# Performance work log

Hardware: AMD Instinct MI355X
Metric: run time of the kernel (lower is better)

## Reference

```python
import jax, jax.numpy as jnp
import numpy as np

BN_EPS = 1e-5

def setup_inputs() -> dict:
    key = jax.random.key(0)
    ks = jax.random.split(key, 6)
    N, D, H = 1024, 256, 128
    scale = 0.05
    return {
        "graph_embeddings": jax.random.normal(ks[0], (N, D), jnp.float32),
        "W1": jax.random.normal(ks[1], (2 * D, H), jnp.float32) * scale,
        "b1": jnp.zeros((H,), jnp.float32),
        "W2": jax.random.normal(ks[2], (H, 1), jnp.float32) * scale,
        "b2": jnp.zeros((1,), jnp.float32),
        "Wg": jax.random.normal(ks[3], (D, H), jnp.float32) * scale,
        "bg": jnp.zeros((H,), jnp.float32),
        "gamma": jnp.ones((H,), jnp.float32),
        "beta": jnp.zeros((H,), jnp.float32),
    }

def reference(graph_embeddings, W1, b1, W2, b2, Wg, bg, gamma, beta):
    N, D = graph_embeddings.shape
    # Pairwise similarity MLP: sim(i,j) = sigmoid(W2 @ relu(W1 @ [x_i; x_j] + b1) + b2)
    # Split W1 over the concat dim so we never materialize [N,N,2D].
    a = graph_embeddings @ W1[:D]          # [N, H] contribution of x_i
    c = graph_embeddings @ W1[D:]          # [N, H] contribution of x_j
    h = jax.nn.relu(a[:, None, :] + c[None, :, :] + b1)   # [N, N, H]
    sim = jax.nn.sigmoid(jnp.einsum('ijh,h->ij', h, W2[:, 0]) + b2[0])  # [N, N]
    # Torch loop uses sim(i,j) with i<j for both directions; keep edge iff sim > 0.5.
    U = jnp.triu(sim, k=1)
    A = jnp.where(U > 0.5, U, 0.0)
    A = A + A.T + jnp.eye(N, dtype=sim.dtype)  # symmetric + GCN self-loops (weight 1)
    # GCN symmetric normalization: D^{-1/2} A D^{-1/2}
    deg = A.sum(axis=1)
    dis = jax.lax.rsqrt(deg)
    A_hat = A * dis[:, None] * dis[None, :]
    out = A_hat @ (graph_embeddings @ Wg) + bg  # [N, H]
    # BatchNorm1d (training mode: batch stats, biased variance)
    mean = out.mean(axis=0)
    var = out.var(axis=0)
    out = gamma * (out - mean) * jax.lax.rsqrt(var + BN_EPS) + beta
    return jax.nn.relu(out)
```

## Files before the change

### kernel.cpp

```cpp
#include <hip/hip_runtime.h>
#include <math.h>

constexpr int NN = 1024;
constexpr int DD = 256;
constexpr int HH = 128;
constexpr float BN_EPS = 1e-5f;

constexpr int OFF_A      = 0;
constexpr int OFF_AP     = OFF_A + NN * NN;
constexpr int OFF_CP     = OFF_AP + NN * HH;
constexpr int OFF_Y      = OFF_CP + NN * HH;
constexpr int OFF_DEG    = OFF_Y + NN * HH;
constexpr int OFF_STATS  = OFF_DEG + NN;
constexpr int OFF_OUTPRE = OFF_STATS + 256;

__global__ __launch_bounds__(256) void k1_gemm(
    const float* __restrict__ X, const float* __restrict__ W1,
    const float* __restrict__ Wg, const float* __restrict__ b1,
    float* __restrict__ aP, float* __restrict__ cP, float* __restrict__ Y,
    float* __restrict__ deg, float* __restrict__ stats) {
  const int tid = threadIdx.x;
  const int blk = blockIdx.x;
  if (blk >= 192) {
    if (blk == 192) {
      for (int i = tid; i < NN; i += 256) deg[i] = 0.f;
    } else {
      stats[tid] = 0.f;
    }
    return;
  }
  __shared__ float xs[16 * 256];
  __shared__ float ws[64 * 128];
  const int i0 = (blk & 63) * 16;
  const int m = blk >> 6;
  const float* W = (m == 0) ? W1 : (m == 1 ? W1 + DD * HH : Wg);
  const float* Xbase = X + i0 * DD;
#pragma unroll
  for (int v = 0; v < 4; ++v) {
    const int fi = (v * 256 + tid) * 4;
    *(float4*)(xs + fi) = *(const float4*)(Xbase + fi);
  }
  const int tx = tid & 31, ty = tid >> 5;
  float4 acc0 = make_float4(0.f, 0.f, 0.f, 0.f);
  float4 acc1 = make_float4(0.f, 0.f, 0.f, 0.f);
  for (int c = 0; c < 4; ++c) {
    __syncthreads();
    const float* Wbase = W + c * 64 * HH;
#pragma unroll
    for (int v = 0; v < 8; ++v) {
      const int fi = (v * 256 + tid) * 4;
      *(float4*)(ws + fi) = *(const float4*)(Wbase + fi);
    }
    __syncthreads();
    const float* xr0 = xs + (ty * 2) * 256 + c * 64;
    const float* xr1 = xs + (ty * 2 + 1) * 256 + c * 64;
#pragma unroll 4
    for (int d = 0; d < 64; d += 4) {
      const float4 x0 = *(const float4*)(xr0 + d);
      const float4 x1 = *(const float4*)(xr1 + d);
      const float4 w0 = *(const float4*)(ws + (d + 0) * 128 + tx * 4);
      const float4 w1 = *(const float4*)(ws + (d + 1) * 128 + tx * 4);
      const float4 w2 = *(const float4*)(ws + (d + 2) * 128 + tx * 4);
      const float4 w3 = *(const float4*)(ws + (d + 3) * 128 + tx * 4);
      acc0.x = fmaf(x0.x, w0.x, acc0.x); acc0.y = fmaf(x0.x, w0.y, acc0.y);
      acc0.z = fmaf(x0.x, w0.z, acc0.z); acc0.w = fmaf(x0.x, w0.w, acc0.w);
      acc1.x = fmaf(x1.x, w0.x, acc1.x); acc1.y = fmaf(x1.x, w0.y, acc1.y);
      acc1.z = fmaf(x1.x, w0.z, acc1.z); acc1.w = fmaf(x1.x, w0.w, acc1.w);
      acc0.x = fmaf(x0.y, w1.x, acc0.x); acc0.y = fmaf(x0.y, w1.y, acc0.y);
      acc0.z = fmaf(x0.y, w1.z, acc0.z); acc0.w = fmaf(x0.y, w1.w, acc0.w);
      acc1.x = fmaf(x1.y, w1.x, acc1.x); acc1.y = fmaf(x1.y, w1.y, acc1.y);
      acc1.z = fmaf(x1.y, w1.z, acc1.z); acc1.w = fmaf(x1.y, w1.w, acc1.w);
      acc0.x = fmaf(x0.z, w2.x, acc0.x); acc0.y = fmaf(x0.z, w2.y, acc0.y);
      acc0.z = fmaf(x0.z, w2.z, acc0.z); acc0.w = fmaf(x0.z, w2.w, acc0.w);
      acc1.x = fmaf(x1.z, w2.x, acc1.x); acc1.y = fmaf(x1.z, w2.y, acc1.y);
      acc1.z = fmaf(x1.z, w2.z, acc1.z); acc1.w = fmaf(x1.z, w2.w, acc1.w);
      acc0.x = fmaf(x0.w, w3.x, acc0.x); acc0.y = fmaf(x0.w, w3.y, acc0.y);
      acc0.z = fmaf(x0.w, w3.z, acc0.z); acc0.w = fmaf(x0.w, w3.w, acc0.w);
      acc1.x = fmaf(x1.w, w3.x, acc1.x); acc1.y = fmaf(x1.w, w3.y, acc1.y);
      acc1.z = fmaf(x1.w, w3.z, acc1.z); acc1.w = fmaf(x1.w, w3.w, acc1.w);
    }
  }
  float* dst = (m == 0) ? aP : (m == 1 ? cP : Y);
  if (m == 0) {
    const float4 bv = *(const float4*)(b1 + tx * 4);
    acc0.x += bv.x; acc0.y += bv.y; acc0.z += bv.z; acc0.w += bv.w;
    acc1.x += bv.x; acc1.y += bv.y; acc1.z += bv.z; acc1.w += bv.w;
  }
  const int r0 = i0 + ty * 2;
  *(float4*)(dst + r0 * HH + tx * 4) = acc0;
  *(float4*)(dst + (r0 + 1) * HH + tx * 4) = acc1;
}

__global__ __launch_bounds__(256) void k2_pairwise(
    const float* __restrict__ aP, const float* __restrict__ cP,
    const float* __restrict__ W2, const float* __restrict__ b2,
    float* __restrict__ A, float* __restrict__ deg) {
  __shared__ float as[32 * 132];
  __shared__ float cs[32 * 132];
  __shared__ float es[32 * 33];
  __shared__ float ws2[128];
  const int tid = threadIdx.x;
  int tt = blockIdx.x, ti = 0;
  while (tt >= 32 - ti) { tt -= 32 - ti; ++ti; }
  const int tj = ti + tt;
  const int i0 = ti * 32, j0 = tj * 32;
  if (tid < 32) *(float4*)(ws2 + tid * 4) = *(const float4*)(W2 + tid * 4);
  for (int idx = tid; idx < 32 * HH; idx += 256) {
    const int row = idx >> 7, col = idx & 127;
    as[row * 132 + col] = aP[(i0 + row) * HH + col];
    cs[row * 132 + col] = cP[(j0 + row) * HH + col];
  }
  __syncthreads();
  const int li0 = (tid >> 4) * 2, lj0 = (tid & 15) * 2;
  float s00 = 0.f, s01 = 0.f, s10 = 0.f, s11 = 0.f;
#pragma unroll 8
  for (int h = 0; h < HH; h += 4) {
    const float4 a0 = *(const float4*)(as + li0 * 132 + h);
    const float4 a1 = *(const float4*)(as + (li0 + 1) * 132 + h);
    const float4 c0 = *(const float4*)(cs + lj0 * 132 + h);
    const float4 c1 = *(const float4*)(cs + (lj0 + 1) * 132 + h);
    const float4 w = *(const float4*)(ws2 + h);
    s00 += fmaxf(a0.x + c0.x, 0.f) * w.x + fmaxf(a0.y + c0.y, 0.f) * w.y +
           fmaxf(a0.z + c0.z, 0.f) * w.z + fmaxf(a0.w + c0.w, 0.f) * w.w;
    s01 += fmaxf(a0.x + c1.x, 0.f) * w.x + fmaxf(a0.y + c1.y, 0.f) * w.y +
           fmaxf(a0.z + c1.z, 0.f) * w.z + fmaxf(a0.w + c1.w, 0.f) * w.w;
    s10 += fmaxf(a1.x + c0.x, 0.f) * w.x + fmaxf(a1.y + c0.y, 0.f) * w.y +
           fmaxf(a1.z + c0.z, 0.f) * w.z + fmaxf(a1.w + c0.w, 0.f) * w.w;
    s11 += fmaxf(a1.x + c1.x, 0.f) * w.x + fmaxf(a1.y + c1.y, 0.f) * w.y +
           fmaxf(a1.z + c1.z, 0.f) * w.z + fmaxf(a1.w + c1.w, 0.f) * w.w;
  }
  const float b2v = b2[0];
  auto edge = [b2v](float s) {
    s += b2v;
    return s > 0.f ? 1.f / (1.f + __expf(-s)) : 0.f;
  };
  es[(li0 + 0) * 33 + lj0 + 0] = edge(s00);
  es[(li0 + 0) * 33 + lj0 + 1] = edge(s01);
  es[(li0 + 1) * 33 + lj0 + 0] = edge(s10);
  es[(li0 + 1) * 33 + lj0 + 1] = edge(s11);
  __syncthreads();
  if (ti == tj) {
    float f[2][2];
#pragma unroll
    for (int r = 0; r < 2; ++r)
#pragma unroll
      for (int c = 0; c < 2; ++c) {
        const int li = li0 + r, lj = lj0 + c;
        f[r][c] =
            (li == lj) ? 1.f : (li < lj ? es[li * 33 + lj] : es[lj * 33 + li]);
      }
    __syncthreads();
    es[(li0 + 0) * 33 + lj0 + 0] = f[0][0];
    es[(li0 + 0) * 33 + lj0 + 1] = f[0][1];
    es[(li0 + 1) * 33 + lj0 + 0] = f[1][0];
    es[(li0 + 1) * 33 + lj0 + 1] = f[1][1];
    __syncthreads();
  }
  if (tid < 32) {
    float s = 0.f;
#pragma unroll
    for (int c = 0; c < 32; ++c) s += es[tid * 33 + c];
    atomicAdd(deg + i0 + tid, s);
  } else if (tid < 64 && ti != tj) {
    const int c = tid - 32;
    float s = 0.f;
#pragma unroll
    for (int r = 0; r < 32; ++r) s += es[r * 33 + c];
    atomicAdd(deg + j0 + c, s);
  }
#pragma unroll
  for (int r = 0; r < 2; ++r)
#pragma unroll
    for (int c = 0; c < 2; ++c) {
      const int li = li0 + r, lj = lj0 + c;
      A[(i0 + li) * NN + j0 + lj] = es[li * 33 + lj];
      if (ti != tj) A[(j0 + li) * NN + i0 + lj] = es[lj * 33 + li];
    }
}

__global__ __launch_bounds__(256) void k3_spmm(
    const float* __restrict__ A, const float* __restrict__ Y,
    const float* __restrict__ deg, const float* __restrict__ bg,
    float* __restrict__ out_pre, float* __restrict__ stats) {
  __shared__ float As[4 * 1024];
  __shared__ float disl[1024];
  __shared__ float sred[512];
  const int tid = threadIdx.x;
  const int i0 = blockIdx.x * 4;
  const float* Ab = A + i0 * NN;
#pragma unroll
  for (int v = 0; v < 4; ++v) {
    const int fi = (v * 256 + tid) * 4;
    *(float4*)(As + fi) = *(const float4*)(Ab + fi);
  }
  {
    const float4 dv = *(const float4*)(deg + tid * 4);
    float4 r;
    r.x = rsqrtf(dv.x); r.y = rsqrtf(dv.y); r.z = rsqrtf(dv.z); r.w = rsqrtf(dv.w);
    *(float4*)(disl + tid * 4) = r;
  }
  __syncthreads();
  const int h = tid & 127, rg = tid >> 7;
  float acc0 = 0.f, acc1 = 0.f;
  const float* Yh = Y + h;
  const float* Ar0 = As + (rg * 2) * 1024;
  const float* Ar1 = As + (rg * 2 + 1) * 1024;
#pragma unroll 4
  for (int j = 0; j < 1024; j += 4) {
    const float4 dv = *(const float4*)(disl + j);
    const float y0 = Yh[(j + 0) * HH] * dv.x;
    const float y1 = Yh[(j + 1) * HH] * dv.y;
    const float y2 = Yh[(j + 2) * HH] * dv.z;
    const float y3 = Yh[(j + 3) * HH] * dv.w;
    const float4 a0 = *(const float4*)(Ar0 + j);
    const float4 a1 = *(const float4*)(Ar1 + j);
    acc0 = fmaf(a0.x, y0, acc0); acc0 = fmaf(a0.y, y1, acc0);
    acc0 = fmaf(a0.z, y2, acc0); acc0 = fmaf(a0.w, y3, acc0);
    acc1 = fmaf(a1.x, y0, acc1); acc1 = fmaf(a1.y, y1, acc1);
    acc1 = fmaf(a1.z, y2, acc1); acc1 = fmaf(a1.w, y3, acc1);
  }
  const float bgv = bg[h];
  const float v0 = acc0 * disl[i0 + rg * 2] + bgv;
  const float v1 = acc1 * disl[i0 + rg * 2 + 1] + bgv;
  out_pre[(i0 + rg * 2) * HH + h] = v0;
  out_pre[(i0 + rg * 2 + 1) * HH + h] = v1;
  sred[rg * 128 + h] = v0 + v1;
  __syncthreads();
  sred[256 + rg * 128 + h] = v0 * v0 + v1 * v1;
  __syncthreads();
  if (rg == 0) {
    atomicAdd(&stats[h], sred[h] + sred[128 + h]);
    atomicAdd(&stats[128 + h], sred[256 + h] + sred[384 + h]);
  }
}

__global__ __launch_bounds__(256) void k4_bn(
    const float* __restrict__ out_pre, const float* __restrict__ stats,
    const float* __restrict__ gamma, const float* __restrict__ beta,
    float* __restrict__ out) {
  const int idx = blockIdx.x * 256 + threadIdx.x;
  const int h = idx & 127;
  const float mean = stats[h] * (1.f / NN);
  const float var = stats[128 + h] * (1.f / NN) - mean * mean;
  float v = (out_pre[idx] - mean) * rsqrtf(var + BN_EPS);
  v = gamma[h] * v + beta[h];
  out[idx] = fmaxf(v, 0.f);
}

extern "C" void kernel_launch(void* const* d_in, const int* in_sizes, int n_in,
                              void* d_out, int out_size, void* d_ws,
                              size_t ws_size, hipStream_t stream) {
  const float* X = (const float*)d_in[0];
  const float* W1 = (const float*)d_in[1];
  const float* b1 = (const float*)d_in[2];
  const float* W2 = (const float*)d_in[3];
  const float* b2 = (const float*)d_in[4];
  const float* Wg = (const float*)d_in[5];
  const float* bg = (const float*)d_in[6];
  const float* gamma = (const float*)d_in[7];
  const float* beta = (const float*)d_in[8];
  float* out = (float*)d_out;

  float* w = (float*)d_ws;
  float* A = w + OFF_A;
  float* aP = w + OFF_AP;
  float* cP = w + OFF_CP;
  float* Y = w + OFF_Y;
  float* deg = w + OFF_DEG;
  float* stats = w + OFF_STATS;
  float* out_pre = w + OFF_OUTPRE;

  k1_gemm<<<dim3(194), 256, 0, stream>>>(X, W1, Wg, b1, aP, cP, Y, deg, stats);
  k2_pairwise<<<dim3(528), 256, 0, stream>>>(aP, cP, W2, b2, A, deg);
  k3_spmm<<<dim3(256), 256, 0, stream>>>(A, Y, deg, bg, out_pre, stats);
  k4_bn<<<dim3(512), 256, 0, stream>>>(out_pre, stats, gamma, beta, out);
}
```

Before: 127.9 us.

## Restructure SpMM block into split-K register tiles with pre-scaled transposed A

The dense A@Y kernel now stores the 4 A rows transposed in shared memory, pre-multiplied by the column normalization, so the inner loop no longer rescales Y per element. Each thread computes a 4x4 register tile (4 rows × 4 hidden columns) over a 128-wide K slice, loading Y as float4. The 8 partial sums are reduced through shared memory. This is meant to raise FMA-per-load intensity and cut scalar strided Y loads, at the cost of more shared memory and an extra reduction step. The stats reduction also drops one barrier.

Measured after the change: 117.5 us. 8.2% less time.

```diff
diff --git a/kernel.cpp b/kernel.cpp
--- a/kernel.cpp
+++ b/kernel.cpp
@@ -182,55 +182,73 @@
     const float* __restrict__ A, const float* __restrict__ Y,
     const float* __restrict__ deg, const float* __restrict__ bg,
     float* __restrict__ out_pre, float* __restrict__ stats) {
-  __shared__ float As[4 * 1024];
-  __shared__ float disl[1024];
-  __shared__ float sred[512];
+  __shared__ float Ast[NN * 4];
+  __shared__ float disl[NN];
+  __shared__ float red[8 * 520];
+  __shared__ float sm1[256], sm2[256];
   const int tid = threadIdx.x;
   const int i0 = blockIdx.x * 4;
-  const float* Ab = A + i0 * NN;
-#pragma unroll
-  for (int v = 0; v < 4; ++v) {
-    const int fi = (v * 256 + tid) * 4;
-    *(float4*)(As + fi) = *(const float4*)(Ab + fi);
-  }
   {
     const float4 dv = *(const float4*)(deg + tid * 4);
     float4 r;
-    r.x = rsqrtf(dv.x); r.y = rsqrtf(dv.y); r.z = rsqrtf(dv.z); r.w = rsqrtf(dv.w);
+    r.x = rsqrtf(dv.x); r.y = rsqrtf(dv.y);
+    r.z = rsqrtf(dv.z); r.w = rsqrtf(dv.w);
     *(float4*)(disl + tid * 4) = r;
   }
   __syncthreads();
-  const int h = tid & 127, rg = tid >> 7;
-  float acc0 = 0.f, acc1 = 0.f;
-  const float* Yh = Y + h;
-  const float* Ar0 = As + (rg * 2) * 1024;
-  const float* Ar1 = As + (rg * 2 + 1) * 1024;
+  const float* Ab = A + i0 * NN;
+#pragma unroll
+  for (int v = 0; v < 4; ++v) {
+    const int fi = (v * 256 + tid) * 4;
+    const float4 av = *(const float4*)(Ab + fi);
+    const int r = fi >> 10, j = fi & 1023;
+    Ast[(j + 0) * 4 + r] = av.x * disl[j + 0];
+    Ast[(j + 1) * 4 + r] = av.y * disl[j + 1];
+    Ast[(j + 2) * 4 + r] = av.z * disl[j + 2];
+    Ast[(j + 3) * 4 + r] = av.w * disl[j + 3];
+  }
+  __syncthreads();
+  const int tx = tid & 31, ty = tid >> 5;
+  const int jbase = ty * 128;
+  float4 acc[4];
+#pragma unroll
+  for (int r = 0; r < 4; ++r) acc[r] = make_float4(0.f, 0.f, 0.f, 0.f);
+  const float* Yb = Y + jbase * HH + tx * 4;
 #pragma unroll 4
-  for (int j = 0; j < 1024; j += 4) {
-    const float4 dv = *(const float4*)(disl + j);
-    const float y0 = Yh[(j + 0) * HH] * dv.x;
-    const float y1 = Yh[(j + 1) * HH] * dv.y;
-    const float y2 = Yh[(j + 2) * HH] * dv.z;
-    const float y3 = Yh[(j + 3) * HH] * dv.w;
-    const float4 a0 = *(const float4*)(Ar0 + j);
-    const float4 a1 = *(const float4*)(Ar1 + j);
-    acc0 = fmaf(a0.x, y0, acc0); acc0 = fmaf(a0.y, y1, acc0);
-    acc0 = fmaf(a0.z, y2, acc0); acc0 = fmaf(a0.w, y3, acc0);
-    acc1 = fmaf(a1.x, y0, acc1); acc1 = fmaf(a1.y, y1, acc1);
-    acc1 = fmaf(a1.z, y2, acc1); acc1 = fmaf(a1.w, y3, acc1);
+  for (int jj = 0; jj < 128; ++jj) {
+    const float4 yv = *(const float4*)(Yb + jj * HH);
+    const float4 ab = *(const float4*)(Ast + (jbase + jj) * 4);
+    acc[0].x = fmaf(ab.x, yv.x, acc[0].x); acc[0].y = fmaf(ab.x, yv.y, acc[0].y);
+    acc[0].z = fmaf(ab.x, yv.z, acc[0].z); acc[0].w = fmaf(ab.x, yv.w, acc[0].w);
+    acc[1].x = fmaf(ab.y, yv.x, acc[1].x); acc[1].y = fmaf(ab.y, yv.y, acc[1].y);
+    acc[1].z = fmaf(ab.y, yv.z, acc[1].z); acc[1].w = fmaf(ab.y, yv.w, acc[1].w);
+    acc[2].x = fmaf(ab.z, yv.x, acc[2].x); acc[2].y = fmaf(ab.z, yv.y, acc[2].y);
+    acc[2].z = fmaf(ab.z, yv.z, acc[2].z); acc[2].w = fmaf(ab.z, yv.w, acc[2].w);
+    acc[3].x = fmaf(ab.w, yv.x, acc[3].x); acc[3].y = fmaf(ab.w, yv.y, acc[3].y);
+    acc[3].z = fmaf(ab.w, yv.z, acc[3].z); acc[3].w = fmaf(ab.w, yv.w, acc[3].w);
+  }
+#pragma unroll
+  for (int r = 0; r < 4; ++r)
+    *(float4*)(red + ty * 520 + r * 128 + tx * 4) = acc[r];
+  __syncthreads();
+  const int h = tid & 127, rr = tid >> 7;
+  float v0 = 0.f, v1 = 0.f;
+#pragma unroll
+  for (int t = 0; t < 8; ++t) {
+    v0 += red[t * 520 + rr * 128 + h];
+    v1 += red[t * 520 + (rr + 2) * 128 + h];
   }
   const float bgv = bg[h];
-  const float v0 = acc0 * disl[i0 + rg * 2] + bgv;
-  const float v1 = acc1 * disl[i0 + rg * 2 + 1] + bgv;
-  out_pre[(i0 + rg * 2) * HH + h] = v0;
-  out_pre[(i0 + rg * 2 + 1) * HH + h] = v1;
-  sred[rg * 128 + h] = v0 + v1;
-  __syncthreads();
-  sred[256 + rg * 128 + h] = v0 * v0 + v1 * v1;
-  __syncthreads();
-  if (rg == 0) {
-    atomicAdd(&stats[h], sred[h] + sred[128 + h]);
-    atomicAdd(&stats[128 + h], sred[256 + h] + sred[384 + h]);
+  v0 = v0 * disl[i0 + rr] + bgv;
+  v1 = v1 * disl[i0 + rr + 2] + bgv;
+  out_pre[(i0 + rr) * HH + h] = v0;
+  out_pre[(i0 + rr + 2) * HH + h] = v1;
+  sm1[rr * 128 + h] = v0 + v1;
+  sm2[rr * 128 + h] = v0 * v0 + v1 * v1;
+  __syncthreads();
+  if (rr == 0) {
+    atomicAdd(&stats[h], sm1[h] + sm1[128 + h]);
+    atomicAdd(&stats[128 + h], sm2[h] + sm2[128 + h]);
   }
 }
 
```
